# Optimization experiments

Hardware: AMD Instinct MI355X
Metric: run time of the kernel (lower is better)

Reference implementation:

```python
import jax, jax.numpy as jnp
import numpy as np

B, N, H, W = 4, 16, 480, 640
Hf, Wf, C = 120, 160, 128
NUM_CLASSES = 14
NUM_EXPERTS = NUM_CLASSES - 1  # 13 per-class ROI experts
ROI = 14  # ROI-align output resolution


def setup_inputs() -> dict:
    key = jax.random.key(0)
    ks = jax.random.split(key, 20)
    inp = {
        'depth': jax.random.normal(ks[0], (B, 1, H, W), jnp.float32),
        'context': jax.random.normal(ks[1], (B, 192, Hf, Wf), jnp.float32),
        'input_feature_map': jax.random.normal(ks[2], (B, C, Hf, Wf), jnp.float32),
        'bin_num': 64,
        'min_depth': 1,
        'max_depth': 10,
        'masks': jax.random.uniform(ks[3], (B, N, Hf, Wf), jnp.float32),
        'instances': jax.random.uniform(ks[4], (B, N, H, W), jnp.float32),
        'boxes': jax.random.uniform(ks[5], (B, N, 4), jnp.float32),
        'labels': jax.random.randint(ks[6], (B, N), 0, NUM_EXPERTS),
    }
    s = 0.05
    # per-class (expert) parameters, stacked on leading expert axis
    inp['w_conv_s'] = s * jax.random.normal(ks[7], (NUM_EXPERTS, C, C, 3, 3), jnp.float32)
    inp['b_conv_s'] = jnp.zeros((NUM_EXPERTS, C), jnp.float32)
    inp['w_fc'] = s * jax.random.normal(ks[8], (NUM_EXPERTS, 2, C), jnp.float32)
    inp['b_fc'] = jnp.zeros((NUM_EXPERTS, 2), jnp.float32)
    inp['w_conv_c1'] = s * jax.random.normal(ks[9], (NUM_EXPERTS, 64, C, 3, 3), jnp.float32)
    inp['b_conv_c1'] = jnp.zeros((NUM_EXPERTS, 64), jnp.float32)
    inp['w_conv_c2'] = s * jax.random.normal(ks[10], (NUM_EXPERTS, 1, 64, 3, 3), jnp.float32)
    inp['b_conv_c2'] = jnp.zeros((NUM_EXPERTS, 1), jnp.float32)
    return inp


def _boxes_norm(boxes_flat):
    # map raw rand [M,4] -> valid normalized (y1,x1,y2,x2) in [0,1]
    y1 = 0.6 * boxes_flat[:, 0]
    x1 = 0.6 * boxes_flat[:, 1]
    y2 = y1 + 0.1 + 0.3 * boxes_flat[:, 2]
    x2 = x1 + 0.1 + 0.3 * boxes_flat[:, 3]
    return y1, x1, y2, x2


def _roi_align(fmap, batch_idx, boxes_flat, R):
    # fmap [B,C,Hf,Wf] -> [M,C,R,R] bilinear ROI sampling (irregular gather)
    _, _, hf, wf = fmap.shape
    y1, x1, y2, x2 = _boxes_norm(boxes_flat)
    t = (jnp.arange(R, dtype=fmap.dtype) + 0.5) / R
    ys = (y1[:, None] + (y2 - y1)[:, None] * t) * (hf - 1)  # [M,R]
    xs = (x1[:, None] + (x2 - x1)[:, None] * t) * (wf - 1)
    y0 = jnp.clip(jnp.floor(ys).astype(jnp.int32), 0, hf - 2)
    x0 = jnp.clip(jnp.floor(xs).astype(jnp.int32), 0, wf - 2)
    wy = jnp.clip(ys - y0, 0.0, 1.0)[:, :, None, None]   # [M,R,1,1]
    wx = jnp.clip(xs - x0, 0.0, 1.0)[:, None, :, None]   # [M,1,R,1]
    b = batch_idx[:, None, None]
    Y0 = y0[:, :, None]
    X0 = x0[:, None, :]
    def g(dy, dx):
        return fmap[b, :, Y0 + dy, X0 + dx]  # [M,R,R,C]
    out = (g(0, 0) * (1 - wy) * (1 - wx) + g(0, 1) * (1 - wy) * wx
           + g(1, 0) * wy * (1 - wx) + g(1, 1) * wy * wx)
    return jnp.transpose(out, (0, 3, 1, 2))  # [M,C,R,R]


def _conv(x, w, b):
    # x [Cin,R,R], w [Cout,Cin,3,3] -> [Cout,R,R]
    y = jax.lax.conv_general_dilated(x[None], w, (1, 1), 'SAME',
                                     dimension_numbers=('NCHW', 'OIHW', 'NCHW'))[0]
    return y + b[:, None, None]

_conv_v = jax.vmap(_conv)  # per-instance expert conv (per-instance weights)


def reference(depth, context, input_feature_map, bin_num, min_depth, max_depth,
              masks, instances, boxes, labels,
              w_conv_s, b_conv_s, w_fc, b_fc, w_conv_c1, b_conv_c1, w_conv_c2, b_conv_c2):
    b_, n_, h, w = instances.shape
    M = b_ * n_
    lab = labels.reshape(M)
    batch_idx = jnp.repeat(jnp.arange(b_), n_)
    boxes_flat = boxes.reshape(M, 4)

    # shared ROI gather of class-routed instances
    roi = _roi_align(input_feature_map, batch_idx, boxes_flat, ROI)  # [M,C,R,R]

    # hard routing: gather each instance's class-expert weights by label
    hs = jax.nn.relu(_conv_v(roi, w_conv_s[lab], b_conv_s[lab]))     # [M,C,R,R]
    gap = hs.mean(axis=(2, 3))                                        # [M,C]
    ss = jnp.einsum('mc,moc->mo', gap, w_fc[lab]) + b_fc[lab]         # [M,2]
    scale = ss[:, 0].reshape(b_, n_)
    shift = ss[:, 1].reshape(b_, n_)

    h1 = jax.nn.relu(_conv_v(roi, w_conv_c1[lab], b_conv_c1[lab]))    # [M,64,R,R]
    c = _conv_v(h1, w_conv_c2[lab], b_conv_c2[lab])                   # [M,1,R,R]
    canonical = jax.image.resize(c, (M, 1, h, w), method='bilinear')
    canonical = canonical.reshape(b_, n_, h, w)

    # loss_type == 0: relu(.).clamp(min=0.001) == max(., 0.001)
    depth_r = jnp.maximum(canonical * scale[..., None, None] + shift[..., None, None], 0.001)
    return depth_r, canonical, scale, shift
```

## Files before the change

### kernel.cpp

```cpp
#include <hip/hip_runtime.h>


typedef unsigned short bfu;
typedef __attribute__((ext_vector_type(8))) short bf16x8;
typedef __attribute__((ext_vector_type(4))) float f32x4;

__device__ __forceinline__ float bf2f(bfu u) {
  union { unsigned int i; float f; } v;
  v.i = ((unsigned int)u) << 16;
  return v.f;
}
__device__ __forceinline__ bfu f2bf(float f) {
  union { float f; unsigned int i; } v;
  v.f = f;
  unsigned int u = v.i;
  u = (u + 0x7fffu + ((u >> 16) & 1u)) >> 16;
  return (bfu)u;
}

#define B_  4
#define N_  16
#define M_  64
#define H_  480
#define W_  640
#define HF  120
#define WF  160
#define C_  128
#define R_  14
#define PIX 196
#define NE  13
#define KK  1152

#define WS_XB    0
#define WS_XH    802816
#define WS_C     1204224
#define WS_GAP   1216768
#define WS_SCALE 1224960
#define WS_SHIFT 1225024
#define WS_WF    1225088
#define WS_BIASF 2662784
#define WS_W2    2665280
#define WS_B2    2672768
#define WS_WFC   2672784
#define WS_BFC   2676112

__global__ __launch_bounds__(256) void prep_kernel(
    const float* __restrict__ w_s, const float* __restrict__ b_s,
    const float* __restrict__ w_fc, const float* __restrict__ b_fc,
    const float* __restrict__ w_c1, const float* __restrict__ b_c1,
    const float* __restrict__ w_c2, const float* __restrict__ b_c2,
    float* __restrict__ ws)
{
  const int P0 = NE*192*KK;
  const int P1 = NE*192;
  const int P2 = NE*576;
  const int P3 = NE;
  const int P4 = NE*256;
  const int P5 = NE*2;
  const int P6 = M_*C_;
  int total = P0+P1+P2+P3+P4+P5+P6;
  bfu* wf = (bfu*)(ws + WS_WF);
  for (int idx = blockIdx.x*256 + threadIdx.x; idx < total; idx += gridDim.x*256) {
    int d = idx;
    if (d < P0) {
      int e = d / (192*KK);
      int r = d - e*(192*KK);
      int oc = r / KK;
      int k  = r - oc*KK;
      int kidx = k >> 7, ic = k & 127;
      float v = (oc < 128) ? w_s[((e*128 + oc)*128 + ic)*9 + kidx]
                           : w_c1[((e*64 + (oc-128))*128 + ic)*9 + kidx];
      wf[d] = f2bf(v);
      continue;
    }
    d -= P0;
    if (d < P1) {
      int e = d / 192, oc = d - e*192;
      ws[WS_BIASF + d] = (oc < 128) ? b_s[e*128 + oc] : b_c1[e*64 + oc - 128];
      continue;
    }
    d -= P1;
    if (d < P2) {
      int e = d / 576, k = d - e*576;
      int kidx = k >> 6, ic = k & 63;
      ws[WS_W2 + d] = w_c2[(e*64 + ic)*9 + kidx];
      continue;
    }
    d -= P2;
    if (d < P3) { ws[WS_B2 + d] = b_c2[d]; continue; }
    d -= P3;
    if (d < P4) { ws[WS_WFC + d] = w_fc[d]; continue; }
    d -= P4;
    if (d < P5) { ws[WS_BFC + d] = b_fc[d]; continue; }
    d -= P5;
    ws[WS_GAP + d] = 0.f;
  }
}

__global__ __launch_bounds__(256) void xb_kernel(
    const float* __restrict__ fmap, const float* __restrict__ boxes,
    float* __restrict__ ws)
{
  __shared__ int iy0[R_], ix0[R_];
  __shared__ float swy[R_], swx[R_];
  int m = blockIdx.x;
  int tid = threadIdx.x;
  if (tid < 2*R_) {
    int r = tid % R_;
    bool isY = tid < R_;
    float b0 = boxes[m*4 + (isY ? 0 : 1)];
    float b2 = boxes[m*4 + (isY ? 2 : 3)];
    float lo = 0.6f * b0;
    float hi = lo + 0.1f + 0.3f * b2;
    float t = ((float)r + 0.5f) / (float)R_;
    float dim = isY ? (float)(HF-1) : (float)(WF-1);
    float s = (lo + (hi - lo) * t) * dim;
    int maxi = isY ? (HF-2) : (WF-2);
    int i0 = (int)floorf(s);
    i0 = i0 < 0 ? 0 : (i0 > maxi ? maxi : i0);
    float w = s - (float)i0;
    w = w < 0.f ? 0.f : (w > 1.f ? 1.f : w);
    if (isY) { iy0[r] = i0; swy[r] = w; } else { ix0[r] = i0; swx[r] = w; }
  }
  __syncthreads();
  int bi = m / N_;
  const float* fb = fmap + (size_t)bi * C_ * HF * WF;
  bfu* xb = (bfu*)(ws + WS_XB);
  for (int idx = tid; idx < PIX*64; idx += 256) {
    int ic2 = (idx & 63) * 2;
    int p = idx >> 6;
    int ry = p / R_, rx = p - (p/R_)*R_;
    int y0 = iy0[ry], x0 = ix0[rx];
    float wy = swy[ry], wx = swx[rx];
    float w00 = (1.f-wy)*(1.f-wx), w01 = (1.f-wy)*wx;
    float w10 = wy*(1.f-wx),       w11 = wy*wx;
    bfu pk[2];
    #pragma unroll
    for (int u = 0; u < 2; ++u) {
      const float* f = fb + ((size_t)(ic2+u)*HF + y0)*WF + x0;
      float v = f[0]*w00 + f[1]*w01 + f[WF]*w10 + f[WF+1]*w11;
      pk[u] = f2bf(v);
    }
    *(ushort2*)&xb[((size_t)m*PIX + p)*128 + ic2] = make_ushort2(pk[0], pk[1]);
  }
}

__global__ __launch_bounds__(256) void gemm_kernel(
    const int* __restrict__ labels, float* __restrict__ ws)
{
  __shared__ bfu lA[128*32];
  __shared__ bfu lB[128*32];
  const bfu* Xb = (const bfu*)(ws + WS_XB);
  const bfu* WFp = (const bfu*)(ws + WS_WF);
  const float* biasf = ws + WS_BIASF;
  float* gap = ws + WS_GAP;
  bfu* Xh = (bfu*)(ws + WS_XH);

  int bx = blockIdx.x;
  int m  = bx >> 2;
  int mb = (bx >> 1) & 1;
  int nb = bx & 1;
  int e = labels[m];
  int tid = threadIdx.x;
  int wave = tid >> 6, lane = tid & 63;
  int wm = wave >> 1, wn = wave & 1;
  int l15 = lane & 15, q = lane >> 4;

  int row0 = tid >> 2, row1 = row0 + 64;
  int kc = tid & 3;
  int loff0 = row0*32 + (kc ^ ((row0 >> 1) & 3))*8;
  int loff1 = row1*32 + (kc ^ ((row1 >> 1) & 3))*8;
  int g0 = mb*128 + row0, g1 = mb*128 + row1;
  bool av0 = g0 < 192, av1 = g1 < 192;
  const bfu* wfe = WFp + (size_t)e*192*KK;
  const bfu* wr0 = wfe + (size_t)g0*KK + kc*8;
  const bfu* wr1 = wfe + (size_t)g1*KK + kc*8;
  int pg0 = nb*128 + row0, pg1 = nb*128 + row1;
  int py0 = pg0 / 14, px0 = pg0 - (pg0/14)*14;
  int py1 = pg1 / 14, px1 = pg1 - (pg1/14)*14;
  bool pv0 = pg0 < PIX, pv1 = pg1 < PIX;
  const bfu* xbm = Xb + (size_t)m*PIX*128;

  f32x4 acc[4][4];
  #pragma unroll
  for (int i = 0; i < 4; ++i)
    #pragma unroll
    for (int j = 0; j < 4; ++j)
      acc[i][j] = (f32x4){0.f, 0.f, 0.f, 0.f};

  const uint4 z4 = make_uint4(0,0,0,0);
  for (int s = 0; s < 36; ++s) {
    int kidx = s >> 2, icc = s & 3;
    int dy = kidx/3 - 1, dx = (kidx - (kidx/3)*3) - 1;
    uint4 a0 = av0 ? *(const uint4*)(wr0 + s*32) : z4;
    uint4 a1 = av1 ? *(const uint4*)(wr1 + s*32) : z4;
    int ys0 = py0 + dy, xs0 = px0 + dx;
    int ys1 = py1 + dy, xs1 = px1 + dx;
    bool v0 = pv0 && (unsigned)ys0 < 14u && (unsigned)xs0 < 14u;
    bool v1 = pv1 && (unsigned)ys1 < 14u && (unsigned)xs1 < 14u;
    uint4 b0 = v0 ? *(const uint4*)(xbm + (size_t)(ys0*14+xs0)*128 + icc*32 + kc*8) : z4;
    uint4 b1 = v1 ? *(const uint4*)(xbm + (size_t)(ys1*14+xs1)*128 + icc*32 + kc*8) : z4;
    __syncthreads();
    *(uint4*)&lA[loff0] = a0;
    *(uint4*)&lA[loff1] = a1;
    *(uint4*)&lB[loff0] = b0;
    *(uint4*)&lB[loff1] = b1;
    __syncthreads();
    bf16x8 af[4], bfr[4];
    #pragma unroll
    for (int i = 0; i < 4; ++i) {
      int r = wm*64 + i*16 + l15;
      af[i] = *(const bf16x8*)&lA[r*32 + (q ^ ((r >> 1) & 3))*8];
    }
    #pragma unroll
    for (int j = 0; j < 4; ++j) {
      int r = wn*64 + j*16 + l15;
      bfr[j] = *(const bf16x8*)&lB[r*32 + (q ^ ((r >> 1) & 3))*8];
    }
    #pragma unroll
    for (int i = 0; i < 4; ++i)
      #pragma unroll
      for (int j = 0; j < 4; ++j)
        acc[i][j] = __builtin_amdgcn_mfma_f32_16x16x32_bf16(af[i], bfr[j], acc[i][j], 0, 0, 0);
  }

  if (mb == 0) {
    #pragma unroll
    for (int i = 0; i < 4; ++i) {
      int ocb = wm*64 + i*16 + q*4;
      f32x4 bv = *(const f32x4*)&biasf[e*192 + ocb];
      #pragma unroll
      for (int r = 0; r < 4; ++r) {
        float sum = 0.f;
        #pragma unroll
        for (int j = 0; j < 4; ++j) {
          int p = nb*128 + wn*64 + j*16 + l15;
          float v = acc[i][j][r] + bv[r];
          v = v > 0.f ? v : 0.f;
          if (p < PIX) sum += v;
        }
        sum += __shfl_xor(sum, 1);
        sum += __shfl_xor(sum, 2);
        sum += __shfl_xor(sum, 4);
        sum += __shfl_xor(sum, 8);
        if (l15 == 0) atomicAdd(&gap[m*C_ + ocb + r], sum);
      }
    }
  } else if (wm == 0) {
    #pragma unroll
    for (int i = 0; i < 4; ++i) {
      int icb = i*16 + q*4;
      f32x4 bv = *(const f32x4*)&biasf[e*192 + 128 + icb];
      #pragma unroll
      for (int j = 0; j < 4; ++j) {
        int p = nb*128 + wn*64 + j*16 + l15;
        if (p < PIX) {
          ushort4 pk;
          float v0 = acc[i][j][0] + bv[0]; v0 = v0 > 0.f ? v0 : 0.f;
          float v1 = acc[i][j][1] + bv[1]; v1 = v1 > 0.f ? v1 : 0.f;
          float v2 = acc[i][j][2] + bv[2]; v2 = v2 > 0.f ? v2 : 0.f;
          float v3 = acc[i][j][3] + bv[3]; v3 = v3 > 0.f ? v3 : 0.f;
          pk.x = f2bf(v0); pk.y = f2bf(v1); pk.z = f2bf(v2); pk.w = f2bf(v3);
          *(ushort4*)&Xh[((size_t)m*PIX + p)*64 + icb] = pk;
        }
      }
    }
  }
}

__global__ __launch_bounds__(128) void fc_kernel(
    const int* __restrict__ labels, float* __restrict__ ws,
    float* __restrict__ out)
{
  int t = threadIdx.x;
  int m = t >> 1, o = t & 1;
  int e = labels[m];
  const float* g = ws + WS_GAP + m*C_;
  const float* wv = ws + WS_WFC + (e*2 + o)*C_;
  float s = 0.f;
  for (int c = 0; c < C_; ++c) s += g[c] * wv[c];
  s = ws[WS_BFC + e*2 + o] + s * (1.f/(float)PIX);
  size_t base = (size_t)2 * M_ * H_ * W_;
  if (o == 0) { ws[WS_SCALE + m] = s; out[base + m] = s; }
  else        { ws[WS_SHIFT + m] = s; out[base + M_ + m] = s; }
}

__global__ __launch_bounds__(256) void convc2_kernel(
    const int* __restrict__ labels, float* __restrict__ ws)
{
  __shared__ bfu xh[PIX*64];
  __shared__ float w2l[576];
  int m = blockIdx.x;
  int e = labels[m];
  int tid = threadIdx.x;
  const bfu* Xh = (const bfu*)(ws + WS_XH) + (size_t)m*PIX*64;
  for (int i = tid; i < PIX*64/8; i += 256)
    *(uint4*)&xh[i*8] = *(const uint4*)&Xh[i*8];
  for (int i = tid; i < 576; i += 256)
    w2l[i] = ws[WS_W2 + e*576 + i];
  __syncthreads();
  if (tid < PIX) {
    int y = tid / 14, x = tid - (tid/14)*14;
    float acc = 0.f;
    #pragma unroll
    for (int kidx = 0; kidx < 9; ++kidx) {
      int ys = y + kidx/3 - 1, xs = x + (kidx - (kidx/3)*3) - 1;
      if ((unsigned)ys < 14u && (unsigned)xs < 14u) {
        const bfu* xr = xh + (ys*14 + xs)*64;
        const float* wr = w2l + kidx*64;
        #pragma unroll
        for (int cc = 0; cc < 8; ++cc) {
          bf16x8 xv = *(const bf16x8*)&xr[cc*8];
          f32x4 wa = *(const f32x4*)&wr[cc*8];
          f32x4 wb = *(const f32x4*)&wr[cc*8 + 4];
          acc += bf2f((bfu)xv[0])*wa[0] + bf2f((bfu)xv[1])*wa[1]
               + bf2f((bfu)xv[2])*wa[2] + bf2f((bfu)xv[3])*wa[3]
               + bf2f((bfu)xv[4])*wb[0] + bf2f((bfu)xv[5])*wb[1]
               + bf2f((bfu)xv[6])*wb[2] + bf2f((bfu)xv[7])*wb[3];
        }
      }
    }
    ws[WS_C + m*PIX + tid] = acc + ws[WS_B2 + e];
  }
}

__global__ __launch_bounds__(256) void resize_kernel(
    const float* __restrict__ ws_c, const float* __restrict__ ws_scale,
    const float* __restrict__ ws_shift, float* __restrict__ out)
{
  __shared__ float cs[PIX];
  int bx = blockIdx.x;
  int m = bx / 150;
  int chunk = bx % 150;
  int tid = threadIdx.x;
  if (tid < PIX) cs[tid] = ws_c[m*PIX + tid];
  __syncthreads();
  float sc = ws_scale[m], sh = ws_shift[m];
  int q0 = chunk*2048 + tid*8;
  int y = q0 / W_;
  int x0i = q0 - y*W_;
  float py = ((float)y + 0.5f) * (14.f/(float)H_) - 0.5f;
  py = fminf(fmaxf(py, 0.f), 13.f);
  int y0 = (int)py; y0 = y0 > 12 ? 12 : y0;
  float wy = py - (float)y0;
  const float* r0 = cs + y0*R_;
  const float* r1 = r0 + R_;
  float vd[8], vc[8];
  #pragma unroll
  for (int u = 0; u < 8; ++u) {
    int x = x0i + u;
    float px = ((float)x + 0.5f) * (14.f/(float)W_) - 0.5f;
    px = fminf(fmaxf(px, 0.f), 13.f);
    int xq = (int)px; xq = xq > 12 ? 12 : xq;
    float wx = px - (float)xq;
    float v = (r0[xq]*(1.f-wx) + r0[xq+1]*wx) * (1.f-wy)
            + (r1[xq]*(1.f-wx) + r1[xq+1]*wx) * wy;
    vc[u] = v;
    vd[u] = fmaxf(v*sc + sh, 0.001f);
  }
  size_t base = (size_t)m * H_ * W_ + q0;
  float* od = out + base;
  float* oc = out + (size_t)M_*H_*W_ + base;
  *(float4*)(od)     = make_float4(vd[0], vd[1], vd[2], vd[3]);
  *(float4*)(od + 4) = make_float4(vd[4], vd[5], vd[6], vd[7]);
  *(float4*)(oc)     = make_float4(vc[0], vc[1], vc[2], vc[3]);
  *(float4*)(oc + 4) = make_float4(vc[4], vc[5], vc[6], vc[7]);
}

extern "C" void kernel_launch(void* const* d_in, const int* in_sizes, int n_in,
                              void* d_out, int out_size, void* d_ws, size_t ws_size,
                              hipStream_t stream) {
  const float* fmap  = (const float*)d_in[2];
  const float* boxes = (const float*)d_in[8];
  const int* labels  = (const int*)d_in[9];
  const float* w_s  = (const float*)d_in[10];
  const float* b_s  = (const float*)d_in[11];
  const float* w_fc = (const float*)d_in[12];
  const float* b_fc = (const float*)d_in[13];
  const float* w_c1 = (const float*)d_in[14];
  const float* b_c1 = (const float*)d_in[15];
  const float* w_c2 = (const float*)d_in[16];
  const float* b_c2 = (const float*)d_in[17];
  float* ws = (float*)d_ws;
  float* out = (float*)d_out;

  hipLaunchKernelGGL(prep_kernel, dim3(1024), dim3(256), 0, stream,
                     w_s, b_s, w_fc, b_fc, w_c1, b_c1, w_c2, b_c2, ws);
  hipLaunchKernelGGL(xb_kernel, dim3(M_), dim3(256), 0, stream,
                     fmap, boxes, ws);
  hipLaunchKernelGGL(gemm_kernel, dim3(M_*4), dim3(256), 0, stream,
                     labels, ws);
  hipLaunchKernelGGL(fc_kernel, dim3(1), dim3(128), 0, stream,
                     labels, ws, out);
  hipLaunchKernelGGL(convc2_kernel, dim3(M_), dim3(256), 0, stream,
                     labels, ws);
  hipLaunchKernelGGL(resize_kernel, dim3(M_*150), dim3(256), 0, stream,
                     ws + WS_C, ws + WS_SCALE, ws + WS_SHIFT, out);
}
```

Measured before the change: 390.9 us.

## Fuse prep with ROI gather, retile conv GEMM to 64-row M tiles, merge fc into convc2

Merges the weight-prep and ROI-align gather into one launch by giving extra blocks to the gather. The gather is rewritten so each thread handles one pixel across all channels with 16-byte stores. The conv GEMM now uses 64-row output-channel tiles, giving 6 blocks per instance instead of 4. This drops the padded rows of the 192-channel dimension and improves occupancy via launch bounds. The fc reduction moves into the convc2 kernel's idle threads to remove a serial one-block launch. The gather now reads fmap with a strided, per-channel pattern across threads, which may coalesce worse.

```diff
diff --git a/kernel.cpp b/kernel.cpp
--- a/kernel.cpp
+++ b/kernel.cpp
@@ -44,111 +44,111 @@
 #define WS_WFC   2672784
 #define WS_BFC   2676112
 
-__global__ __launch_bounds__(256) void prep_kernel(
+#define PREP_BLK 1024
+
+__global__ __launch_bounds__(256) void prep_xb_kernel(
+    const float* __restrict__ fmap, const float* __restrict__ boxes,
     const float* __restrict__ w_s, const float* __restrict__ b_s,
     const float* __restrict__ w_fc, const float* __restrict__ b_fc,
     const float* __restrict__ w_c1, const float* __restrict__ b_c1,
     const float* __restrict__ w_c2, const float* __restrict__ b_c2,
     float* __restrict__ ws)
 {
-  const int P0 = NE*192*KK;
-  const int P1 = NE*192;
-  const int P2 = NE*576;
-  const int P3 = NE;
-  const int P4 = NE*256;
-  const int P5 = NE*2;
-  const int P6 = M_*C_;
-  int total = P0+P1+P2+P3+P4+P5+P6;
-  bfu* wf = (bfu*)(ws + WS_WF);
-  for (int idx = blockIdx.x*256 + threadIdx.x; idx < total; idx += gridDim.x*256) {
-    int d = idx;
-    if (d < P0) {
-      int e = d / (192*KK);
-      int r = d - e*(192*KK);
-      int oc = r / KK;
-      int k  = r - oc*KK;
-      int kidx = k >> 7, ic = k & 127;
-      float v = (oc < 128) ? w_s[((e*128 + oc)*128 + ic)*9 + kidx]
-                           : w_c1[((e*64 + (oc-128))*128 + ic)*9 + kidx];
-      wf[d] = f2bf(v);
-      continue;
-    }
-    d -= P0;
-    if (d < P1) {
-      int e = d / 192, oc = d - e*192;
-      ws[WS_BIASF + d] = (oc < 128) ? b_s[e*128 + oc] : b_c1[e*64 + oc - 128];
-      continue;
-    }
-    d -= P1;
-    if (d < P2) {
-      int e = d / 576, k = d - e*576;
-      int kidx = k >> 6, ic = k & 63;
-      ws[WS_W2 + d] = w_c2[(e*64 + ic)*9 + kidx];
-      continue;
-    }
-    d -= P2;
-    if (d < P3) { ws[WS_B2 + d] = b_c2[d]; continue; }
-    d -= P3;
-    if (d < P4) { ws[WS_WFC + d] = w_fc[d]; continue; }
-    d -= P4;
-    if (d < P5) { ws[WS_BFC + d] = b_fc[d]; continue; }
-    d -= P5;
-    ws[WS_GAP + d] = 0.f;
-  }
-}
-
-__global__ __launch_bounds__(256) void xb_kernel(
-    const float* __restrict__ fmap, const float* __restrict__ boxes,
-    float* __restrict__ ws)
-{
-  __shared__ int iy0[R_], ix0[R_];
-  __shared__ float swy[R_], swx[R_];
-  int m = blockIdx.x;
   int tid = threadIdx.x;
-  if (tid < 2*R_) {
-    int r = tid % R_;
-    bool isY = tid < R_;
-    float b0 = boxes[m*4 + (isY ? 0 : 1)];
-    float b2 = boxes[m*4 + (isY ? 2 : 3)];
-    float lo = 0.6f * b0;
-    float hi = lo + 0.1f + 0.3f * b2;
-    float t = ((float)r + 0.5f) / (float)R_;
-    float dim = isY ? (float)(HF-1) : (float)(WF-1);
-    float s = (lo + (hi - lo) * t) * dim;
-    int maxi = isY ? (HF-2) : (WF-2);
-    int i0 = (int)floorf(s);
-    i0 = i0 < 0 ? 0 : (i0 > maxi ? maxi : i0);
-    float w = s - (float)i0;
-    w = w < 0.f ? 0.f : (w > 1.f ? 1.f : w);
-    if (isY) { iy0[r] = i0; swy[r] = w; } else { ix0[r] = i0; swx[r] = w; }
+  if (blockIdx.x < PREP_BLK) {
+    const int P0 = NE*192*KK;
+    const int P1 = NE*192;
+    const int P2 = NE*576;
+    const int P3 = NE;
+    const int P4 = NE*256;
+    const int P5 = NE*2;
+    const int P6 = M_*C_;
+    int total = P0+P1+P2+P3+P4+P5+P6;
+    bfu* wf = (bfu*)(ws + WS_WF);
+    for (int idx = blockIdx.x*256 + tid; idx < total; idx += PREP_BLK*256) {
+      int d = idx;
+      if (d < P0) {
+        int e = d / (192*KK);
+        int r = d - e*(192*KK);
+        int oc = r / KK;
+        int k  = r - oc*KK;
+        int kidx = k >> 7, ic = k & 127;
+        float v = (oc < 128) ? w_s[((e*128 + oc)*128 + ic)*9 + kidx]
+                             : w_c1[((e*64 + (oc-128))*128 + ic)*9 + kidx];
+        wf[d] = f2bf(v);
+        continue;
+      }
+      d -= P0;
+      if (d < P1) {
+        int e = d / 192, oc = d - e*192;
+        ws[WS_BIASF + d] = (oc < 128) ? b_s[e*128 + oc] : b_c1[e*64 + oc - 128];
+        continue;
+      }
+      d -= P1;
+      if (d < P2) {
+        int e = d / 576, k = d - e*576;
+        int kidx = k >> 6, ic = k & 63;
+        ws[WS_W2 + d] = w_c2[(e*64 + ic)*9 + kidx];
+        continue;
+      }
+      d -= P2;
+      if (d < P3) { ws[WS_B2 + d] = b_c2[d]; continue; }
+      d -= P3;
+      if (d < P4) { ws[WS_WFC + d] = w_fc[d]; continue; }
+      d -= P4;
+      if (d < P5) { ws[WS_BFC + d] = b_fc[d]; continue; }
+      d -= P5;
+      ws[WS_GAP + d] = 0.f;
+    }
+    return;
+  }
+
+  int m = blockIdx.x - PREP_BLK;
+  __shared__ int sy0[PIX], sx0[PIX];
+  __shared__ float s00[PIX], s01[PIX], s10[PIX], s11[PIX];
+  if (tid < PIX) {
+    int p = tid;
+    int ry = p / R_, rx = p - ry*R_;
+    float by1 = boxes[m*4+0], bx1 = boxes[m*4+1];
+    float by2 = boxes[m*4+2], bx2 = boxes[m*4+3];
+    float ylo = 0.6f*by1, yhi = ylo + 0.1f + 0.3f*by2;
+    float xlo = 0.6f*bx1, xhi = xlo + 0.1f + 0.3f*bx2;
+    float ty = ((float)ry + 0.5f) / (float)R_;
+    float tx = ((float)rx + 0.5f) / (float)R_;
+    float sy = (ylo + (yhi-ylo)*ty) * (float)(HF-1);
+    float sx = (xlo + (xhi-xlo)*tx) * (float)(WF-1);
+    int y0 = (int)floorf(sy); y0 = y0 < 0 ? 0 : (y0 > HF-2 ? HF-2 : y0);
+    int x0 = (int)floorf(sx); x0 = x0 < 0 ? 0 : (x0 > WF-2 ? WF-2 : x0);
+    float wy = sy - (float)y0; wy = wy < 0.f ? 0.f : (wy > 1.f ? 1.f : wy);
+    float wx = sx - (float)x0; wx = wx < 0.f ? 0.f : (wx > 1.f ? 1.f : wx);
+    sy0[p] = y0; sx0[p] = x0;
+    s00[p] = (1.f-wy)*(1.f-wx); s01[p] = (1.f-wy)*wx;
+    s10[p] = wy*(1.f-wx);       s11[p] = wy*wx;
   }
   __syncthreads();
-  int bi = m / N_;
-  const float* fb = fmap + (size_t)bi * C_ * HF * WF;
-  bfu* xb = (bfu*)(ws + WS_XB);
-  for (int idx = tid; idx < PIX*64; idx += 256) {
-    int ic2 = (idx & 63) * 2;
-    int p = idx >> 6;
-    int ry = p / R_, rx = p - (p/R_)*R_;
-    int y0 = iy0[ry], x0 = ix0[rx];
-    float wy = swy[ry], wx = swx[rx];
-    float w00 = (1.f-wy)*(1.f-wx), w01 = (1.f-wy)*wx;
-    float w10 = wy*(1.f-wx),       w11 = wy*wx;
-    bfu pk[2];
-    #pragma unroll
-    for (int u = 0; u < 2; ++u) {
-      const float* f = fb + ((size_t)(ic2+u)*HF + y0)*WF + x0;
+  if (tid >= PIX) return;
+  int p = tid;
+  const float* fb = fmap + (size_t)(m / N_) * C_ * HF * WF
+                  + (size_t)sy0[p]*WF + sx0[p];
+  float w00 = s00[p], w01 = s01[p], w10 = s10[p], w11 = s11[p];
+  bfu* xbp = (bfu*)(ws + WS_XB) + ((size_t)m*PIX + p)*128;
+  #pragma unroll 2
+  for (int icb = 0; icb < 16; ++icb) {
+    bfu pk[8];
+    #pragma unroll
+    for (int u = 0; u < 8; ++u) {
+      const float* f = fb + (size_t)(icb*8 + u)*HF*WF;
       float v = f[0]*w00 + f[1]*w01 + f[WF]*w10 + f[WF+1]*w11;
       pk[u] = f2bf(v);
     }
-    *(ushort2*)&xb[((size_t)m*PIX + p)*128 + ic2] = make_ushort2(pk[0], pk[1]);
-  }
-}
-
-__global__ __launch_bounds__(256) void gemm_kernel(
+    *(uint4*)&xbp[icb*8] = *(uint4*)pk;
+  }
+}
+
+__global__ __launch_bounds__(256, 2) void gemm_kernel(
     const int* __restrict__ labels, float* __restrict__ ws)
 {
-  __shared__ bfu lA[128*32];
+  __shared__ bfu lA[64*32];
   __shared__ bfu lB[128*32];
   const bfu* Xb = (const bfu*)(ws + WS_XB);
   const bfu* WFp = (const bfu*)(ws + WS_WF);
@@ -157,33 +157,32 @@
   bfu* Xh = (bfu*)(ws + WS_XH);
 
   int bx = blockIdx.x;
-  int m  = bx >> 2;
-  int mb = (bx >> 1) & 1;
-  int nb = bx & 1;
+  int m  = bx / 6;
+  int r6 = bx - m*6;
+  int mb = r6 >> 1;
+  int nb = r6 & 1;
   int e = labels[m];
   int tid = threadIdx.x;
   int wave = tid >> 6, lane = tid & 63;
   int wm = wave >> 1, wn = wave & 1;
   int l15 = lane & 15, q = lane >> 4;
 
-  int row0 = tid >> 2, row1 = row0 + 64;
-  int kc = tid & 3;
-  int loff0 = row0*32 + (kc ^ ((row0 >> 1) & 3))*8;
-  int loff1 = row1*32 + (kc ^ ((row1 >> 1) & 3))*8;
-  int g0 = mb*128 + row0, g1 = mb*128 + row1;
-  bool av0 = g0 < 192, av1 = g1 < 192;
-  const bfu* wfe = WFp + (size_t)e*192*KK;
-  const bfu* wr0 = wfe + (size_t)g0*KK + kc*8;
-  const bfu* wr1 = wfe + (size_t)g1*KK + kc*8;
-  int pg0 = nb*128 + row0, pg1 = nb*128 + row1;
-  int py0 = pg0 / 14, px0 = pg0 - (pg0/14)*14;
-  int py1 = pg1 / 14, px1 = pg1 - (pg1/14)*14;
-  bool pv0 = pg0 < PIX, pv1 = pg1 < PIX;
+  int arow = tid >> 2, kc = tid & 3;
+  const bfu* wr = WFp + (size_t)e*192*KK + (size_t)(mb*64 + arow)*KK + kc*8;
+  int aoff = arow*32 + (kc ^ ((arow >> 1) & 3))*8;
+
+  int brow0 = tid >> 2, brow1 = brow0 + 64;
+  int boff0 = brow0*32 + (kc ^ ((brow0 >> 1) & 3))*8;
+  int boff1 = brow1*32 + (kc ^ ((brow1 >> 1) & 3))*8;
+  int pg0 = nb*128 + brow0, pg1 = nb*128 + brow1;
+  int py0 = pg0 / 14, px0 = pg0 - py0*14;
+  int py1 = pg1 / 14, px1 = pg1 - py1*14;
+  bool pv1 = pg1 < PIX;
   const bfu* xbm = Xb + (size_t)m*PIX*128;
 
-  f32x4 acc[4][4];
+  f32x4 acc[2][4];
   #pragma unroll
-  for (int i = 0; i < 4; ++i)
+  for (int i = 0; i < 2; ++i)
     #pragma unroll
     for (int j = 0; j < 4; ++j)
       acc[i][j] = (f32x4){0.f, 0.f, 0.f, 0.f};
@@ -191,51 +190,50 @@
   const uint4 z4 = make_uint4(0,0,0,0);
   for (int s = 0; s < 36; ++s) {
     int kidx = s >> 2, icc = s & 3;
-    int dy = kidx/3 - 1, dx = (kidx - (kidx/3)*3) - 1;
-    uint4 a0 = av0 ? *(const uint4*)(wr0 + s*32) : z4;
-    uint4 a1 = av1 ? *(const uint4*)(wr1 + s*32) : z4;
+    int k3 = kidx / 3;
+    int dy = k3 - 1, dx = (kidx - k3*3) - 1;
+    uint4 a = *(const uint4*)(wr + s*32);
     int ys0 = py0 + dy, xs0 = px0 + dx;
     int ys1 = py1 + dy, xs1 = px1 + dx;
-    bool v0 = pv0 && (unsigned)ys0 < 14u && (unsigned)xs0 < 14u;
+    bool v0 = (unsigned)ys0 < 14u && (unsigned)xs0 < 14u;
     bool v1 = pv1 && (unsigned)ys1 < 14u && (unsigned)xs1 < 14u;
     uint4 b0 = v0 ? *(const uint4*)(xbm + (size_t)(ys0*14+xs0)*128 + icc*32 + kc*8) : z4;
     uint4 b1 = v1 ? *(const uint4*)(xbm + (size_t)(ys1*14+xs1)*128 + icc*32 + kc*8) : z4;
     __syncthreads();
-    *(uint4*)&lA[loff0] = a0;
-    *(uint4*)&lA[loff1] = a1;
-    *(uint4*)&lB[loff0] = b0;
-    *(uint4*)&lB[loff1] = b1;
+    *(uint4*)&lA[aoff] = a;
+    *(uint4*)&lB[boff0] = b0;
+    *(uint4*)&lB[boff1] = b1;
     __syncthreads();
-    bf16x8 af[4], bfr[4];
-    #pragma unroll
-    for (int i = 0; i < 4; ++i) {
-      int r = wm*64 + i*16 + l15;
-      af[i] = *(const bf16x8*)&lA[r*32 + (q ^ ((r >> 1) & 3))*8];
+    bf16x8 af[2], bfr[4];
+    #pragma unroll
+    for (int i = 0; i < 2; ++i) {
+      int rr = wm*32 + i*16 + l15;
+      af[i] = *(const bf16x8*)&lA[rr*32 + (q ^ ((rr >> 1) & 3))*8];
     }
     #pragma unroll
     for (int j = 0; j < 4; ++j) {
-      int r = wn*64 + j*16 + l15;
-      bfr[j] = *(const bf16x8*)&lB[r*32 + (q ^ ((r >> 1) & 3))*8];
-    }
-    #pragma unroll
-    for (int i = 0; i < 4; ++i)
+      int rr = wn*64 + j*16 + l15;
+      bfr[j] = *(const bf16x8*)&lB[rr*32 + (q ^ ((rr >> 1) & 3))*8];
+    }
+    #pragma unroll
+    for (int i = 0; i < 2; ++i)
       #pragma unroll
       for (int j = 0; j < 4; ++j)
         acc[i][j] = __builtin_amdgcn_mfma_f32_16x16x32_bf16(af[i], bfr[j], acc[i][j], 0, 0, 0);
   }
 
-  if (mb == 0) {
-    #pragma unroll
-    for (int i = 0; i < 4; ++i) {
-      int ocb = wm*64 + i*16 + q*4;
+  if (mb < 2) {
+    #pragma unroll
+    for (int i = 0; i < 2; ++i) {
+      int ocb = mb*64 + wm*32 + i*16 + q*4;
       f32x4 bv = *(const f32x4*)&biasf[e*192 + ocb];
       #pragma unroll
-      for (int r = 0; r < 4; ++r) {
+      for (int rr = 0; rr < 4; ++rr) {
         float sum = 0.f;
         #pragma unroll
         for (int j = 0; j < 4; ++j) {
           int p = nb*128 + wn*64 + j*16 + l15;
-          float v = acc[i][j][r] + bv[r];
+          float v = acc[i][j][rr] + bv[rr];
           v = v > 0.f ? v : 0.f;
           if (p < PIX) sum += v;
         }
@@ -243,13 +241,13 @@
         sum += __shfl_xor(sum, 2);
         sum += __shfl_xor(sum, 4);
         sum += __shfl_xor(sum, 8);
-        if (l15 == 0) atomicAdd(&gap[m*C_ + ocb + r], sum);
-      }
-    }
-  } else if (wm == 0) {
-    #pragma unroll
-    for (int i = 0; i < 4; ++i) {
-      int icb = i*16 + q*4;
+        if (l15 == 0) atomicAdd(&gap[m*C_ + ocb + rr], sum);
+      }
+    }
+  } else {
+    #pragma unroll
+    for (int i = 0; i < 2; ++i) {
+      int icb = wm*32 + i*16 + q*4;
       f32x4 bv = *(const f32x4*)&biasf[e*192 + 128 + icb];
       #pragma unroll
       for (int j = 0; j < 4; ++j) {
@@ -268,25 +266,9 @@
   }
 }
 
-__global__ __launch_bounds__(128) void fc_kernel(
+__global__ __launch_bounds__(256) void convc2_fc_kernel(
     const int* __restrict__ labels, float* __restrict__ ws,
     float* __restrict__ out)
-{
-  int t = threadIdx.x;
-  int m = t >> 1, o = t & 1;
-  int e = labels[m];
-  const float* g = ws + WS_GAP + m*C_;
-  const float* wv = ws + WS_WFC + (e*2 + o)*C_;
-  float s = 0.f;
-  for (int c = 0; c < C_; ++c) s += g[c] * wv[c];
-  s = ws[WS_BFC + e*2 + o] + s * (1.f/(float)PIX);
-  size_t base = (size_t)2 * M_ * H_ * W_;
-  if (o == 0) { ws[WS_SCALE + m] = s; out[base + m] = s; }
-  else        { ws[WS_SHIFT + m] = s; out[base + M_ + m] = s; }
-}
-
-__global__ __launch_bounds__(256) void convc2_kernel(
-    const int* __restrict__ labels, float* __restrict__ ws)
 {
   __shared__ bfu xh[PIX*64];
   __shared__ float w2l[576];
@@ -321,6 +303,24 @@
       }
     }
     ws[WS_C + m*PIX + tid] = acc + ws[WS_B2 + e];
+  } else if (tid >= 208 && tid < 240) {
+    int o = (tid - 208) >> 4;
+    int g16 = (tid - 208) & 15;
+    const float* g = ws + WS_GAP + m*C_ + g16*8;
+    const float* wv = ws + WS_WFC + (e*2 + o)*C_ + g16*8;
+    float s = 0.f;
+    #pragma unroll
+    for (int c = 0; c < 8; ++c) s += g[c] * wv[c];
+    s += __shfl_xor(s, 1);
+    s += __shfl_xor(s, 2);
+    s += __shfl_xor(s, 4);
+    s += __shfl_xor(s, 8);
+    if (g16 == 0) {
+      s = ws[WS_BFC + e*2 + o] + s * (1.f/(float)PIX);
+      size_t base = (size_t)2 * M_ * H_ * W_;
+      if (o == 0) { ws[WS_SCALE + m] = s; out[base + m] = s; }
+      else        { ws[WS_SHIFT + m] = s; out[base + M_ + m] = s; }
+    }
   }
 }
 
@@ -384,16 +384,12 @@
   float* ws = (float*)d_ws;
   float* out = (float*)d_out;
 
-  hipLaunchKernelGGL(prep_kernel, dim3(1024), dim3(256), 0, stream,
-                     w_s, b_s, w_fc, b_fc, w_c1, b_c1, w_c2, b_c2, ws);
-  hipLaunchKernelGGL(xb_kernel, dim3(M_), dim3(256), 0, stream,
-                     fmap, boxes, ws);
-  hipLaunchKernelGGL(gemm_kernel, dim3(M_*4), dim3(256), 0, stream,
+  hipLaunchKernelGGL(prep_xb_kernel, dim3(PREP_BLK + M_), dim3(256), 0, stream,
+                     fmap, boxes, w_s, b_s, w_fc, b_fc, w_c1, b_c1, w_c2, b_c2, ws);
+  hipLaunchKernelGGL(gemm_kernel, dim3(M_*6), dim3(256), 0, stream,
                      labels, ws);
-  hipLaunchKernelGGL(fc_kernel, dim3(1), dim3(128), 0, stream,
+  hipLaunchKernelGGL(convc2_fc_kernel, dim3(M_), dim3(256), 0, stream,
                      labels, ws, out);
-  hipLaunchKernelGGL(convc2_kernel, dim3(M_), dim3(256), 0, stream,
-                     labels, ws);
   hipLaunchKernelGGL(resize_kernel, dim3(M_*150), dim3(256), 0, stream,
                      ws + WS_C, ws + WS_SCALE, ws + WS_SHIFT, out);
 }
```

After: 407.7 us. 4.3% more time.
